# Performance work log

Hardware: AMD Instinct MI355X
Metric: run time of the kernel (lower is better)

Reference implementation:

```python
import jax, jax.numpy as jnp
import numpy as np

NUM_HEADS = 8
NUM_GROUPS = 32
EPS = 1e-5
RESCALE = 1.0


def setup_inputs() -> dict:
    key = jax.random.key(0)
    ks = jax.random.split(key, 7)
    b, c, h, w = 16, 512, 32, 32
    return {
        "x": jax.random.normal(ks[0], (b, c, h, w), jnp.float32),
        "norm_w": jax.random.normal(ks[1], (c,), jnp.float32),
        "norm_b": jax.random.normal(ks[2], (c,), jnp.float32),
        "qkv_w": jax.random.normal(ks[3], (3 * c, c), jnp.float32) * (c ** -0.5),
        "qkv_b": jax.random.normal(ks[4], (3 * c,), jnp.float32) * 0.02,
        "proj_w": jax.random.normal(ks[5], (c, c), jnp.float32) * (c ** -0.5),
        "proj_b": jax.random.normal(ks[6], (c,), jnp.float32) * 0.02,
    }


def _group_norm(x, w, b):
    # x: [B, C, L]
    B, C, L = x.shape
    g = x.reshape(B, NUM_GROUPS, (C // NUM_GROUPS) * L)
    mu = jnp.mean(g, axis=-1, keepdims=True)
    var = jnp.var(g, axis=-1, keepdims=True)
    g = (g - mu) * jax.lax.rsqrt(var + EPS)
    return g.reshape(B, C, L) * w[None, :, None] + b[None, :, None]


def reference(x, norm_w, norm_b, qkv_w, qkv_b, proj_w, proj_b):
    b, c, hh, ww = x.shape
    L = hh * ww
    H = NUM_HEADS
    ch = c // H  # head dim

    xr = x.reshape(b, c, L)
    hid = _group_norm(xr, norm_w, norm_b)

    # 1x1 conv1d == matmul over channel dim: [3c, c] @ [b, c, L]
    qkv = jnp.einsum('oc,bcl->bol', qkv_w, hid) + qkv_b[None, :, None]
    # torch: reshape(b*H, 3*ch, L).split(ch) -> per-head contiguous [q|k|v] blocks
    qkv = qkv.reshape(b, H, 3, ch, L)
    q, k, v = qkv[:, :, 0], qkv[:, :, 1], qkv[:, :, 2]  # [b, H, ch, L]

    scale = 1.0 / (ch ** 0.25)
    weight = jnp.einsum('bhct,bhcs->bhts', q * scale, k * scale)
    weight = jax.nn.softmax(weight.astype(jnp.float32), axis=-1).astype(weight.dtype)
    a = jnp.einsum('bhts,bhcs->bhct', weight, v)  # [b, H, ch, L]

    h = a.reshape(b, c, L)
    h = jnp.einsum('oc,bcl->bol', proj_w, h) + proj_b[None, :, None]
    h = h.reshape(b, c, hh, ww)
    return (x + h) / RESCALE
```

## Files before the change

### kernel.cpp

```cpp
#include <hip/hip_runtime.h>
#include <hip/hip_bf16.h>
#include <stdint.h>


using f32x4  = __attribute__((ext_vector_type(4))) float;
using bf16x8 = __attribute__((ext_vector_type(8))) __bf16;
using s8v    = __attribute__((ext_vector_type(8))) short;
using s4v    = __attribute__((ext_vector_type(4))) short;

__device__ __forceinline__ short f2bf(float f){
  union { float f; unsigned u; } c; c.f = f;
  unsigned r = (c.u + 0x7FFFu + ((c.u >> 16) & 1u)) >> 16;
  return (short)r;
}

__device__ __forceinline__ float exp2_fast(float x){
#if __has_builtin(__builtin_amdgcn_exp2f)
  return __builtin_amdgcn_exp2f(x);
#else
  return exp2f(x);
#endif
}

__device__ __forceinline__ void gl_lds16(const void* g, void* l){
  __builtin_amdgcn_global_load_lds((const __attribute__((address_space(1))) void*)g,
                                   (__attribute__((address_space(3))) void*)l, 16, 0, 0);
}

__global__ void k_convw(const float* __restrict__ qw, const float* __restrict__ pw,
                        const float* __restrict__ qb,
                        short* __restrict__ qwb, short* __restrict__ pwb,
                        float* __restrict__ qbp){
  int i = blockIdx.x * 256 + threadIdx.x;
  if (i < 786432){
    int o = i >> 9, kk = i & 511;
    int h = o / 192, rem = o - h*192;
    int nr = (rem >> 6)*512 + h*64 + (rem & 63);
    qwb[nr*512 + kk] = f2bf(qw[i]);
  } else if (i < 1048576){
    int j = i - 786432;
    pwb[j] = f2bf(pw[j]);
  } else if (i < 1050112){
    int o = i - 1048576;
    int h = o / 192, rem = o - h*192;
    qbp[(rem >> 6)*512 + h*64 + (rem & 63)] = qb[o];
  }
}

__global__ __launch_bounds__(256) void k_gnorm(const float* __restrict__ x,
                                               const float* __restrict__ w,
                                               const float* __restrict__ bia,
                                               short* __restrict__ hid){
  int b = blockIdx.x >> 5;
  int g = blockIdx.x & 31;
  int tid = threadIdx.x;
  const float* xg = x + ((size_t)b*512 + g*16)*1024;
  int l0 = tid * 4;
  float v[16][4];
  float s1 = 0.f, s2 = 0.f;
  #pragma unroll
  for (int c = 0; c < 16; c++){
    f32x4 t = *(const f32x4*)(xg + c*1024 + l0);
    #pragma unroll
    for (int j = 0; j < 4; j++){ v[c][j] = t[j]; s1 += t[j]; s2 += t[j]*t[j]; }
  }
  #pragma unroll
  for (int m = 32; m; m >>= 1){ s1 += __shfl_xor(s1, m); s2 += __shfl_xor(s2, m); }
  __shared__ float r1[4], r2[4];
  int wv = tid >> 6, ln = tid & 63;
  if (ln == 0){ r1[wv] = s1; r2[wv] = s2; }
  __syncthreads();
  s1 = r1[0]+r1[1]+r1[2]+r1[3];
  s2 = r2[0]+r2[1]+r2[2]+r2[3];
  float mu = s1 * (1.f/16384.f);
  float var = s2 * (1.f/16384.f) - mu*mu;
  float rs = rsqrtf(var + 1e-5f);
  float ww[16], bb[16];
  #pragma unroll
  for (int c = 0; c < 16; c++){ ww[c] = w[g*16+c]*rs; bb[c] = bia[g*16+c]; }
  #pragma unroll
  for (int j = 0; j < 4; j++){
    short o[16];
    #pragma unroll
    for (int c = 0; c < 16; c++) o[c] = f2bf((v[c][j]-mu)*ww[c] + bb[c]);
    short* dst = hid + ((size_t)(b*1024 + l0 + j))*512 + g*16;
    *(s8v*)dst     = *(s8v*)o;
    *(s8v*)(dst+8) = *(s8v*)(o+8);
  }
}

template<int EPI>
__global__ __launch_bounds__(256) void k_gemm(
    const short* __restrict__ A, const short* __restrict__ Bm,
    const float* __restrict__ bias, const float* __restrict__ xres,
    short* __restrict__ q_t, short* __restrict__ k_t, short* __restrict__ v_t,
    float* __restrict__ outp)
{
  __shared__ short Lds[16384];
  int id = blockIdx.x;
  int xcd = id & 7, ix = id >> 3;
  int mt, nt;
  if (EPI == 0){ mt = ix % 12; nt = ix / 12; }
  else         { mt = ix & 3;  nt = ix >> 2; }
  int m0 = mt * 128;
  int n0 = (xcd + 8*nt) * 128;
  int tid = threadIdx.x;
  int lane = tid & 63;
  int wv = tid >> 6;
  int wr = wv >> 1, wc = wv & 1;
  int l15 = lane & 15, g = lane >> 4;
  f32x4 acc[4][4] = {};

  auto STAGE = [&](int db, int t){
    int k0 = t * 32;
    #pragma unroll
    for (int i = 0; i < 4; i++){
      int cc = wv*4 + i;
      int c2 = cc & 7;
      int row = c2*16 + (lane>>2), slot = lane & 3;
      const short* src = (cc < 8 ? A + (size_t)(m0+row)*512
                                 : Bm + (size_t)(n0+row)*512)
                         + k0 + ((slot ^ ((row>>1)&3))*8);
      char* dst = (char*)Lds + db*16384 + (cc < 8 ? 0 : 8192) + c2*1024;
      gl_lds16(src, dst);
    }
  };

  auto COMPUTE = [&](int db){
    const char* Ab = (const char*)Lds + db*16384;
    const char* Bb = Ab + 8192;
    bf16x8 af[4], bf[4];
    #pragma unroll
    for (int m = 0; m < 4; m++){
      int row = wr*64 + m*16 + l15;
      af[m] = *(const bf16x8*)(Ab + row*64 + ((g*16) ^ (((row>>1)&3)<<4)));
    }
    #pragma unroll
    for (int n = 0; n < 4; n++){
      int row = wc*64 + n*16 + l15;
      bf[n] = *(const bf16x8*)(Bb + row*64 + ((g*16) ^ (((row>>1)&3)<<4)));
    }
    __builtin_amdgcn_s_setprio(1);
    #pragma unroll
    for (int m = 0; m < 4; m++)
      #pragma unroll
      for (int n = 0; n < 4; n++)
        acc[m][n] = __builtin_amdgcn_mfma_f32_16x16x32_bf16(af[m], bf[n], acc[m][n], 0, 0, 0);
    __builtin_amdgcn_s_setprio(0);
  };

  STAGE(0, 0);
  for (int t = 0; t < 16; t++){
    asm volatile("s_waitcnt vmcnt(0)" ::: "memory");
    __builtin_amdgcn_s_barrier();
    if (t < 15) STAGE((t+1)&1, t+1);
    COMPUTE(t&1);
  }
  __builtin_amdgcn_s_barrier();

  if (EPI == 0){
    int sel = m0 >> 9;
    if (sel < 2){
      const float sc = (sel == 0) ? 0.18033688011112042f : 1.0f;
      short* dstb = (sel == 0) ? q_t : k_t;
      #pragma unroll
      for (int m = 0; m < 4; m++){
        int ob = m0 + wr*64 + m*16 + (g<<2);
        int hh = (ob>>6)&7, c0 = ob&63;
        float bs[4];
        #pragma unroll
        for (int r = 0; r < 4; r++) bs[r] = bias[ob+r];
        #pragma unroll
        for (int n = 0; n < 4; n++){
          int nn = n0 + wc*64 + n*16 + l15;
          int bb = nn >> 10, ll = nn & 1023;
          int bh = bb*8 + hh;
          short o4[4];
          #pragma unroll
          for (int r = 0; r < 4; r++) o4[r] = f2bf((acc[m][n][r] + bs[r]) * sc);
          *(s4v*)(dstb + ((size_t)bh*1024 + ll)*64 + c0) = *(s4v*)o4;
        }
      }
    } else {
      short* Sc = Lds;
      #pragma unroll
      for (int m = 0; m < 4; m++){
        int ob = m0 + wr*64 + m*16 + (g<<2);
        int h2 = (ob>>6)&1, cq = (ob>>4)&3;
        float bs[4];
        #pragma unroll
        for (int r = 0; r < 4; r++) bs[r] = bias[ob+r];
        #pragma unroll
        for (int n = 0; n < 4; n++){
          int nn = n0 + wc*64 + n*16 + l15;
          int sl = nn & 63, sreg = (nn>>6)&1;
          int ks2 = sl >> 5, gq = (sl>>2)&3, i2 = (sl&3) + 4*((sl>>4)&1);
          int base = (h2*2 + sreg)*4096 + (((ks2*4+gq)*4 + cq)*16 + (g<<2))*8 + i2;
          #pragma unroll
          for (int r = 0; r < 4; r++)
            Sc[base + r*8] = f2bf(acc[m][n][r] + bs[r]);
        }
      }
      __syncthreads();
      int b0  = n0 >> 10;
      int s64 = (n0 >> 6) & 15;
      int hb  = (m0 - 1024) >> 6;
      #pragma unroll
      for (int it = 0; it < 8; it++){
        int flat = it*2048 + tid*8;
        int h2 = flat >> 13, rem = flat & 8191, sreg = rem >> 12, off = rem & 4095;
        int bh = b0*8 + hb + h2;
        *(s8v*)(v_t + ((size_t)bh*16 + s64 + sreg)*4096 + off) = *(const s8v*)(Sc + flat);
      }
    }
  } else {
    #pragma unroll
    for (int m = 0; m < 4; m++){
      int ob = m0 + wr*64 + m*16 + (g<<2);
      float bs[4];
      #pragma unroll
      for (int r = 0; r < 4; r++) bs[r] = bias[ob+r];
      #pragma unroll
      for (int n = 0; n < 4; n++){
        int nn = n0 + wc*64 + n*16 + l15;
        int bb = nn >> 10, ll = nn & 1023;
        #pragma unroll
        for (int r = 0; r < 4; r++){
          size_t idx = ((size_t)bb*512 + ob + r)*1024 + ll;
          outp[idx] = xres[idx] + acc[m][n][r] + bs[r];
        }
      }
    }
  }
}

__global__ __launch_bounds__(256, 4) void k_attn(
    const short* __restrict__ q_t, const short* __restrict__ k_t,
    const short* __restrict__ v_t, short* __restrict__ a_bt)
{
  __shared__ short Kh[4*2048];
  __shared__ short Vh[4*2048];
  int id = blockIdx.x;
  int xcd = id & 7, ix = id >> 3;
  int bh = xcd*16 + (ix >> 3);
  int qb = ix & 7;
  int bb = bh >> 3, hh = bh & 7;
  int tid = threadIdx.x;
  int lane = tid & 63;
  int wv = tid >> 6;
  int l15 = lane & 15, g = lane >> 4;

  bf16x8 qf[2][2];
  #pragma unroll
  for (int qt = 0; qt < 2; qt++){
    const short* qbase = q_t + ((size_t)bh*1024 + qb*128 + qt*64 + wv*16 + l15)*64 + g*8;
    qf[qt][0] = *(const bf16x8*)(qbase);
    qf[qt][1] = *(const bf16x8*)(qbase + 32);
  }
  asm volatile("" :: "v"(qf[0][0]), "v"(qf[0][1]), "v"(qf[1][0]), "v"(qf[1][1]));

  bf16x8 onesb;
  #pragma unroll
  for (int i = 0; i < 8; i++) onesb[i] = (__bf16)1.0f;

  f32x4 o[2][4] = {};
  f32x4 osum[2] = {};

  auto STAGE = [&](int db, int h){
    int t64 = h >> 1, ks = h & 1;
    #pragma unroll
    for (int i = 0; i < 2; i++){
      int cc = wv*2 + i;
      if (cc < 4){
        int row = cc*8 + (lane>>3), slot = lane & 7;
        gl_lds16(k_t + ((size_t)bh*1024 + h*32 + row)*64 + ((slot ^ (row&7))*8),
                 (char*)Kh + db*4096 + cc*1024);
      } else {
        gl_lds16(v_t + ((size_t)bh*16 + t64)*4096 + ks*2048 + (cc-4)*512 + lane*8,
                 (char*)Vh + db*4096 + (cc-4)*1024);
      }
    }
  };

  auto COMPUTE = [&](int db){
    const char* Kb = (const char*)Kh + db*4096;
    const char* Vb = (const char*)Vh + db*4096;
    f32x4 scl[2][2] = {};
    #pragma unroll
    for (int jl = 0; jl < 2; jl++){
      int row = jl*16 + l15;
      int swz = (row&7)<<4;
      bf16x8 kf0 = *(const bf16x8*)(Kb + row*128 + ((g*16) ^ swz));
      bf16x8 kf1 = *(const bf16x8*)(Kb + row*128 + ((64 + g*16) ^ swz));
      __builtin_amdgcn_s_setprio(1);
      #pragma unroll
      for (int qt = 0; qt < 2; qt++){
        scl[qt][jl] = __builtin_amdgcn_mfma_f32_16x16x32_bf16(kf0, qf[qt][0], scl[qt][jl], 0, 0, 0);
        scl[qt][jl] = __builtin_amdgcn_mfma_f32_16x16x32_bf16(kf1, qf[qt][1], scl[qt][jl], 0, 0, 0);
      }
      __builtin_amdgcn_s_setprio(0);
    }
    bf16x8 pa[2];
    #pragma unroll
    for (int qt = 0; qt < 2; qt++){
      #pragma unroll
      for (int i2 = 0; i2 < 8; i2++)
        pa[qt][i2] = (__bf16)exp2_fast(scl[qt][i2>>2][i2&3]);
      osum[qt] = __builtin_amdgcn_mfma_f32_16x16x32_bf16(pa[qt], onesb, osum[qt], 0, 0, 0);
    }
    #pragma unroll
    for (int jd = 0; jd < 4; jd++){
      bf16x8 vbb = *(const bf16x8*)(Vb + (g*4+jd)*256 + l15*16);
      __builtin_amdgcn_s_setprio(1);
      #pragma unroll
      for (int qt = 0; qt < 2; qt++)
        o[qt][jd] = __builtin_amdgcn_mfma_f32_16x16x32_bf16(pa[qt], vbb, o[qt][jd], 0, 0, 0);
      __builtin_amdgcn_s_setprio(0);
    }
  };

  STAGE(0, 0);
  STAGE(1, 1);
  #pragma unroll 2
  for (int h = 0; h < 30; h++){
    STAGE((h+2)&3, h+2);
    asm volatile("s_waitcnt vmcnt(4)" ::: "memory");
    __builtin_amdgcn_s_barrier();
    COMPUTE(h&3);
  }
  asm volatile("s_waitcnt vmcnt(2)" ::: "memory");
  __builtin_amdgcn_s_barrier();
  COMPUTE(2);
  asm volatile("s_waitcnt vmcnt(0)" ::: "memory");
  __builtin_amdgcn_s_barrier();
  COMPUTE(3);

  #pragma unroll
  for (int qt = 0; qt < 2; qt++){
    #pragma unroll
    for (int r = 0; r < 4; r++){
      float inv = 1.f / osum[qt][r];
      int qrow = qb*128 + qt*64 + wv*16 + g*4 + r;
      #pragma unroll
      for (int jd = 0; jd < 4; jd++)
        a_bt[((size_t)bb*1024 + qrow)*512 + hh*64 + jd*16 + l15] = f2bf(o[qt][jd][r] * inv);
    }
  }
}

extern "C" void kernel_launch(void* const* d_in, const int* in_sizes, int n_in,
                              void* d_out, int out_size, void* d_ws, size_t ws_size,
                              hipStream_t stream){
  const float* x  = (const float*)d_in[0];
  const float* nw = (const float*)d_in[1];
  const float* nb = (const float*)d_in[2];
  const float* qw = (const float*)d_in[3];
  const float* qb = (const float*)d_in[4];
  const float* pw = (const float*)d_in[5];
  const float* pb = (const float*)d_in[6];
  float* outp = (float*)d_out;

  char* ws = (char*)d_ws;
  short* hid  = (short*)(ws);
  short* qwb  = (short*)(ws + 16777216);
  short* pwb  = (short*)(ws + 18350080);
  short* q_t  = (short*)(ws + 18874368);
  short* k_t  = (short*)(ws + 35651584);
  short* v_t  = (short*)(ws + 52428800);
  short* a_bt = hid;
  float* qbp  = (float*)d_out;
  if (ws_size < 69206016) return;

  k_convw<<<4103, 256, 0, stream>>>(qw, pw, qb, qwb, pwb, qbp);
  k_gnorm<<<512, 256, 0, stream>>>(x, nw, nb, hid);
  k_gemm<0><<<1536, 256, 0, stream>>>(qwb, hid, qbp, nullptr, q_t, k_t, v_t, nullptr);
  k_attn<<<1024, 256, 0, stream>>>(q_t, k_t, v_t, a_bt);
  k_gemm<1><<<512, 256, 0, stream>>>(pwb, a_bt, pb, x, nullptr, nullptr, nullptr, outp);
}
```

Before: 129.2 us.

## Replace LDS-staged GEMM with direct global-to-register loads and wider N tiles

The GEMM kernels drop LDS double buffering and barriers and load A/B fragments straight from global memory into registers for each MFMA step. The N tile doubles to 256, so each wave computes 4x8 accumulators, and the grids are halved to match. The V-transpose epilogue now uses 64KB of dynamic shared memory. This removes the LDS traffic and barrier overhead, but the loads are now strided and uncoalesced across rows with no pipelining. The larger accumulator set also raises register pressure.

```diff
diff --git a/kernel.cpp b/kernel.cpp
--- a/kernel.cpp
+++ b/kernel.cpp
@@ -90,73 +90,47 @@
 }
 
 template<int EPI>
-__global__ __launch_bounds__(256) void k_gemm(
+__global__ __launch_bounds__(256, 2) void k_gemm(
     const short* __restrict__ A, const short* __restrict__ Bm,
     const float* __restrict__ bias, const float* __restrict__ xres,
     short* __restrict__ q_t, short* __restrict__ k_t, short* __restrict__ v_t,
     float* __restrict__ outp)
 {
-  __shared__ short Lds[16384];
+  extern __shared__ short Sc[];
   int id = blockIdx.x;
   int xcd = id & 7, ix = id >> 3;
   int mt, nt;
   if (EPI == 0){ mt = ix % 12; nt = ix / 12; }
   else         { mt = ix & 3;  nt = ix >> 2; }
   int m0 = mt * 128;
-  int n0 = (xcd + 8*nt) * 128;
+  int n0 = (xcd + 8*nt) * 256;
   int tid = threadIdx.x;
   int lane = tid & 63;
   int wv = tid >> 6;
   int wr = wv >> 1, wc = wv & 1;
   int l15 = lane & 15, g = lane >> 4;
-  f32x4 acc[4][4] = {};
-
-  auto STAGE = [&](int db, int t){
-    int k0 = t * 32;
-    #pragma unroll
-    for (int i = 0; i < 4; i++){
-      int cc = wv*4 + i;
-      int c2 = cc & 7;
-      int row = c2*16 + (lane>>2), slot = lane & 3;
-      const short* src = (cc < 8 ? A + (size_t)(m0+row)*512
-                                 : Bm + (size_t)(n0+row)*512)
-                         + k0 + ((slot ^ ((row>>1)&3))*8);
-      char* dst = (char*)Lds + db*16384 + (cc < 8 ? 0 : 8192) + c2*1024;
-      gl_lds16(src, dst);
-    }
-  };
-
-  auto COMPUTE = [&](int db){
-    const char* Ab = (const char*)Lds + db*16384;
-    const char* Bb = Ab + 8192;
-    bf16x8 af[4], bf[4];
-    #pragma unroll
-    for (int m = 0; m < 4; m++){
-      int row = wr*64 + m*16 + l15;
-      af[m] = *(const bf16x8*)(Ab + row*64 + ((g*16) ^ (((row>>1)&3)<<4)));
-    }
-    #pragma unroll
-    for (int n = 0; n < 4; n++){
-      int row = wc*64 + n*16 + l15;
-      bf[n] = *(const bf16x8*)(Bb + row*64 + ((g*16) ^ (((row>>1)&3)<<4)));
-    }
+
+  const short* Ap = A  + (size_t)(m0 + wr*64  + l15)*512 + g*8;
+  const short* Bp = Bm + (size_t)(n0 + wc*128 + l15)*512 + g*8;
+
+  f32x4 acc[4][8] = {};
+  #pragma unroll
+  for (int t = 0; t < 16; t++){
+    bf16x8 af[4], bf[8];
+    #pragma unroll
+    for (int m = 0; m < 4; m++)
+      af[m] = *(const bf16x8*)(Ap + (size_t)m*16*512 + t*32);
+    #pragma unroll
+    for (int n = 0; n < 8; n++)
+      bf[n] = *(const bf16x8*)(Bp + (size_t)n*16*512 + t*32);
     __builtin_amdgcn_s_setprio(1);
     #pragma unroll
     for (int m = 0; m < 4; m++)
       #pragma unroll
-      for (int n = 0; n < 4; n++)
+      for (int n = 0; n < 8; n++)
         acc[m][n] = __builtin_amdgcn_mfma_f32_16x16x32_bf16(af[m], bf[n], acc[m][n], 0, 0, 0);
     __builtin_amdgcn_s_setprio(0);
-  };
-
-  STAGE(0, 0);
-  for (int t = 0; t < 16; t++){
-    asm volatile("s_waitcnt vmcnt(0)" ::: "memory");
-    __builtin_amdgcn_s_barrier();
-    if (t < 15) STAGE((t+1)&1, t+1);
-    COMPUTE(t&1);
-  }
-  __builtin_amdgcn_s_barrier();
+  }
 
   if (EPI == 0){
     int sel = m0 >> 9;
@@ -171,8 +145,8 @@
         #pragma unroll
         for (int r = 0; r < 4; r++) bs[r] = bias[ob+r];
         #pragma unroll
-        for (int n = 0; n < 4; n++){
-          int nn = n0 + wc*64 + n*16 + l15;
+        for (int n = 0; n < 8; n++){
+          int nn = n0 + wc*128 + n*16 + l15;
           int bb = nn >> 10, ll = nn & 1023;
           int bh = bb*8 + hh;
           short o4[4];
@@ -182,7 +156,6 @@
         }
       }
     } else {
-      short* Sc = Lds;
       #pragma unroll
       for (int m = 0; m < 4; m++){
         int ob = m0 + wr*64 + m*16 + (g<<2);
@@ -191,11 +164,11 @@
         #pragma unroll
         for (int r = 0; r < 4; r++) bs[r] = bias[ob+r];
         #pragma unroll
-        for (int n = 0; n < 4; n++){
-          int nn = n0 + wc*64 + n*16 + l15;
-          int sl = nn & 63, sreg = (nn>>6)&1;
+        for (int n = 0; n < 8; n++){
+          int nn = n0 + wc*128 + n*16 + l15;
+          int sl = nn & 63, sreg = (nn>>6)&3;
           int ks2 = sl >> 5, gq = (sl>>2)&3, i2 = (sl&3) + 4*((sl>>4)&1);
-          int base = (h2*2 + sreg)*4096 + (((ks2*4+gq)*4 + cq)*16 + (g<<2))*8 + i2;
+          int base = (h2*4 + sreg)*4096 + (((ks2*4+gq)*4 + cq)*16 + (g<<2))*8 + i2;
           #pragma unroll
           for (int r = 0; r < 4; r++)
             Sc[base + r*8] = f2bf(acc[m][n][r] + bs[r]);
@@ -206,9 +179,10 @@
       int s64 = (n0 >> 6) & 15;
       int hb  = (m0 - 1024) >> 6;
       #pragma unroll
-      for (int it = 0; it < 8; it++){
+      for (int it = 0; it < 16; it++){
         int flat = it*2048 + tid*8;
-        int h2 = flat >> 13, rem = flat & 8191, sreg = rem >> 12, off = rem & 4095;
+        int reg = flat >> 12, off = flat & 4095;
+        int h2 = reg >> 2, sreg = reg & 3;
         int bh = b0*8 + hb + h2;
         *(s8v*)(v_t + ((size_t)bh*16 + s64 + sreg)*4096 + off) = *(const s8v*)(Sc + flat);
       }
@@ -221,8 +195,8 @@
       #pragma unroll
       for (int r = 0; r < 4; r++) bs[r] = bias[ob+r];
       #pragma unroll
-      for (int n = 0; n < 4; n++){
-        int nn = n0 + wc*64 + n*16 + l15;
+      for (int n = 0; n < 8; n++){
+        int nn = n0 + wc*128 + n*16 + l15;
         int bb = nn >> 10, ll = nn & 1023;
         #pragma unroll
         for (int r = 0; r < 4; r++){
@@ -373,7 +347,7 @@
 
   k_convw<<<4103, 256, 0, stream>>>(qw, pw, qb, qwb, pwb, qbp);
   k_gnorm<<<512, 256, 0, stream>>>(x, nw, nb, hid);
-  k_gemm<0><<<1536, 256, 0, stream>>>(qwb, hid, qbp, nullptr, q_t, k_t, v_t, nullptr);
+  k_gemm<0><<<768, 256, 65536, stream>>>(qwb, hid, qbp, nullptr, q_t, k_t, v_t, nullptr);
   k_attn<<<1024, 256, 0, stream>>>(q_t, k_t, v_t, a_bt);
-  k_gemm<1><<<512, 256, 0, stream>>>(pwb, a_bt, pb, x, nullptr, nullptr, nullptr, outp);
-}
+  k_gemm<1><<<256, 256, 0, stream>>>(pwb, a_bt, pb, x, nullptr, nullptr, nullptr, outp);
+}
```

After: 169.3 us. 1.31x slower.
